# Optimization experiments

Measured on AMD Instinct MI355X. Metric: run time of the kernel, lower is better.

Reference implementation:

```python
import jax, jax.numpy as jnp
from jax import lax
import numpy as np

B, C, H, W = 4, 256, 64, 64
CQK = C // 8  # 32


def conv3x3(x, w, b):
    # x: [B,C_in,H,W], w: [C_out,C_in,3,3], b: [C_out]
    y = lax.conv_general_dilated(x, w, window_strides=(1, 1), padding='SAME',
                                 dimension_numbers=('NCHW', 'OIHW', 'NCHW'))
    return y + b[None, :, None, None]


def setup_inputs() -> dict:
    key = jax.random.key(0)
    ks = jax.random.split(key, 8)
    scale = 0.02
    return {
        'x': jax.random.normal(ks[0], (B, C, H, W), dtype=jnp.float32),
        'wq': jax.random.normal(ks[1], (CQK, C, 3, 3), dtype=jnp.float32) * scale,
        'bq': jax.random.normal(ks[2], (CQK,), dtype=jnp.float32) * scale,
        'wk': jax.random.normal(ks[3], (CQK, C, 3, 3), dtype=jnp.float32) * scale,
        'bk': jax.random.normal(ks[4], (CQK,), dtype=jnp.float32) * scale,
        'wv': jax.random.normal(ks[5], (C, C, 3, 3), dtype=jnp.float32) * scale,
        'bv': jax.random.normal(ks[6], (C,), dtype=jnp.float32) * scale,
        'gamma': jax.random.normal(ks[7], (1,), dtype=jnp.float32) * scale,
    }


def reference(x, wq, bq, wk, bk, wv, bv, gamma):
    b, c, h, w = x.shape
    n = h * w
    # Q: [B, N, C//8]  (permute(0,2,1) of the flattened conv output)
    q = conv3x3(x, wq, bq).reshape(b, -1, n).transpose(0, 2, 1)
    # K: [B, C//8, N]
    k = conv3x3(x, wk, bk).reshape(b, -1, n)
    # s: [B, N_q, N_k]
    s = jnp.einsum('bqd,bdk->bqk', q, k)
    # NOTE: original uses Softmax(dim=-2), i.e. over the QUERY axis
    attn_T = jax.nn.softmax(s, axis=-2)
    # V: [B, C, N]
    v = conv3x3(x, wv, bv).reshape(b, c, n)
    # o = bmm(V, attn_T): [B, C, N]
    o = jnp.einsum('bcq,bqk->bck', v, attn_T).reshape(b, c, h, w)
    return x + gamma * o
```

## Files before the change

### kernel.cpp

```cpp
#include <hip/hip_runtime.h>
#include <cstddef>

#define N_PIX 4096
#define HW 64
#define LOG2E 1.4426950408889634f
#define SHIFT2 28.8539008177793f

typedef __attribute__((ext_vector_type(8))) short bf16x8;
typedef __attribute__((ext_vector_type(4))) float f32x4;

static __device__ __forceinline__ unsigned short f2bf(float f) {
    union { float f; unsigned u; } v; v.f = f;
    unsigned r = v.u + 0x7fffu + ((v.u >> 16) & 1u);
    return (unsigned short)(r >> 16);
}
static __device__ __forceinline__ float bf2f(unsigned short s) {
    union { unsigned u; float f; } v; v.u = (unsigned)s << 16;
    return v.f;
}
static __device__ __forceinline__ unsigned pack_bf16_trunc(float lo, float hi) {
    union { float f; unsigned u; } a, b; a.f = hi; b.f = lo;
    return __builtin_amdgcn_perm(a.u, b.u, 0x07060302u);
}

__global__ __launch_bounds__(256) void x_transpose(
    const float* __restrict__ x, unsigned short* __restrict__ xbf)
{
    __shared__ unsigned short Ts[64][72];
    const int tid = threadIdx.x;
    const int px0 = blockIdx.x * 64, ci0 = blockIdx.y * 64, b = blockIdx.z;
    const float* xb = x + ((size_t)b * 256 + ci0) * N_PIX;

#pragma unroll
    for (int r = 0; r < 4; ++r) {
        int c = r * 16 + (tid >> 4);
        int p4 = (tid & 15) * 4;
        float4 v = *(const float4*)&xb[(size_t)c * N_PIX + px0 + p4];
        Ts[c][p4 + 0] = f2bf(v.x);
        Ts[c][p4 + 1] = f2bf(v.y);
        Ts[c][p4 + 2] = f2bf(v.z);
        Ts[c][p4 + 3] = f2bf(v.w);
    }
    __syncthreads();
#pragma unroll
    for (int r = 0; r < 2; ++r) {
        int id = tid * 2 + r;
        int p = id >> 3, c8 = (id & 7) * 8;
        ushort4 lo, hi;
        lo.x = Ts[c8 + 0][p]; lo.y = Ts[c8 + 1][p];
        lo.z = Ts[c8 + 2][p]; lo.w = Ts[c8 + 3][p];
        hi.x = Ts[c8 + 4][p]; hi.y = Ts[c8 + 5][p];
        hi.z = Ts[c8 + 6][p]; hi.w = Ts[c8 + 7][p];
        size_t off = ((size_t)b * N_PIX + px0 + p) * 256 + ci0 + c8;
        *(ushort4*)&xbf[off]     = lo;
        *(ushort4*)&xbf[off + 4] = hi;
    }
}

__global__ __launch_bounds__(256) void w_transform(
    const float* __restrict__ wq, const float* __restrict__ wk,
    const float* __restrict__ wv, unsigned short* __restrict__ wAll)
{
    int gid = blockIdx.x * 256 + threadIdx.x;
    if (gid >= 72 * 320 * 4) return;
    int part = gid & 3;
    int m = (gid >> 2) % 320;
    int kb = gid / 1280;
    int t = kb >> 3;
    int ci0 = (kb & 7) * 32 + part * 8;
    const float* src; int co; float sc = 1.f;
    if (m < 256)      { src = wv; co = m; }
    else if (m < 288) { src = wq; co = m - 256; sc = LOG2E; }
    else              { src = wk; co = m - 288; }
    ushort4 lo, hi;
    lo.x = f2bf(sc * src[((size_t)co * 256 + ci0 + 0) * 9 + t]);
    lo.y = f2bf(sc * src[((size_t)co * 256 + ci0 + 1) * 9 + t]);
    lo.z = f2bf(sc * src[((size_t)co * 256 + ci0 + 2) * 9 + t]);
    lo.w = f2bf(sc * src[((size_t)co * 256 + ci0 + 3) * 9 + t]);
    hi.x = f2bf(sc * src[((size_t)co * 256 + ci0 + 4) * 9 + t]);
    hi.y = f2bf(sc * src[((size_t)co * 256 + ci0 + 5) * 9 + t]);
    hi.z = f2bf(sc * src[((size_t)co * 256 + ci0 + 6) * 9 + t]);
    hi.w = f2bf(sc * src[((size_t)co * 256 + ci0 + 7) * 9 + t]);
    size_t off = ((size_t)kb * 320 + m) * 32 + part * 8;
    *(ushort4*)&wAll[off]     = lo;
    *(ushort4*)&wAll[off + 4] = hi;
}

__global__ __launch_bounds__(512, 2) void conv_gemm_v5(
    const unsigned short* __restrict__ xbf, const unsigned short* __restrict__ wAll,
    const float* __restrict__ bq, const float* __restrict__ bk,
    const float* __restrict__ bv,
    unsigned short* __restrict__ vbf, unsigned short* __restrict__ qt,
    unsigned short* __restrict__ kt)
{
    __shared__ unsigned short Xs[3 * 66 * 136];

    const int tid = threadIdx.x;
    const int w = tid >> 6, lane = tid & 63, quad = lane >> 4, l15 = lane & 15;
    const int y = blockIdx.x;
    const int b = blockIdx.y;
    const int r0 = (w >> 1) * 80;
    const int p0 = (w & 1) * 32;

    const unsigned short* xb = xbf + (size_t)b * N_PIX * 256;
    const unsigned short* aBase = wAll + ((size_t)(r0 + l15) * 32 + quad * 8);

    const int scol = tid >> 3;
    const int sg2  = (tid & 7) * 2;

    bf16x8 S[3][2];
    auto stage_load = [&](int h) {
#pragma unroll
        for (int ry = 0; ry < 3; ++ry) {
            int gy = y + ry - 1;
            if ((unsigned)gy < 64u) {
                const unsigned short* s =
                    xb + ((size_t)(gy * 64 + scol) * 256 + h * 128 + sg2 * 8);
                S[ry][0] = *(const bf16x8*)&s[0];
                S[ry][1] = *(const bf16x8*)&s[8];
            } else {
                S[ry][0] = (bf16x8){0,0,0,0,0,0,0,0};
                S[ry][1] = (bf16x8){0,0,0,0,0,0,0,0};
            }
        }
    };
    auto stage_store = [&]() {
#pragma unroll
        for (int ry = 0; ry < 3; ++ry) {
            *(bf16x8*)&Xs[(ry * 66 + scol + 1) * 136 + sg2 * 8]     = S[ry][0];
            *(bf16x8*)&Xs[(ry * 66 + scol + 1) * 136 + sg2 * 8 + 8] = S[ry][1];
        }
    };

    bf16x8 afA[2][5], afB[2][5];
    auto load_a = [&](int kb, bf16x8 (&af)[2][5]) {
        const unsigned short* p = aBase + (size_t)kb * 10240;
#pragma unroll
        for (int kl = 0; kl < 2; ++kl)
#pragma unroll
            for (int cb = 0; cb < 5; ++cb)
                af[kl][cb] = *(const bf16x8*)&p[kl * 10240 + cb * 512];
    };

    bf16x8 bfA[2][2], bfB[2][2];
    auto load_bf = [&](int t, int q2, bf16x8 (&bf)[2][2]) {
        int ty = t / 3;
        int dx = t - ty * 3 - 1;
#pragma unroll
        for (int kl = 0; kl < 2; ++kl)
#pragma unroll
            for (int jb = 0; jb < 2; ++jb) {
                int sx = p0 + jb * 16 + l15 + dx + 1;
                int cg = q2 * 8 + kl * 4 + quad;
                bf[kl][jb] = *(const bf16x8*)&Xs[(ty * 66 + sx) * 136 + cg * 8];
            }
    };

    f32x4 acc[5][2];
#pragma unroll
    for (int cb = 0; cb < 5; ++cb)
#pragma unroll
        for (int jb = 0; jb < 2; ++jb) acc[cb][jb] = (f32x4){0.f, 0.f, 0.f, 0.f};

    auto mfma_step = [&](bf16x8 (&af)[2][5], bf16x8 (&bf)[2][2]) {
#pragma unroll
        for (int kl = 0; kl < 2; ++kl)
#pragma unroll
            for (int cb = 0; cb < 5; ++cb)
#pragma unroll
                for (int jb = 0; jb < 2; ++jb)
                    acc[cb][jb] = __builtin_amdgcn_mfma_f32_16x16x32_bf16(
                        af[kl][cb], bf[kl][jb], acc[cb][jb], 0, 0, 0);
    };

    stage_load(0);
    load_a(0, afA);
    stage_store();
    if (tid < 96) {
        int ry = tid >> 5, rem = tid & 31;
        int sx = (rem >> 4) ? 65 : 0;
        int cg = rem & 15;
        *(bf16x8*)&Xs[(ry * 66 + sx) * 136 + cg * 8] = (bf16x8){0,0,0,0,0,0,0,0};
    }
    __syncthreads();

    stage_load(1);

    load_bf(0, 0, bfA);
#pragma unroll
    for (int s = 0; s < 18; s += 2) {
        const int t1 = (s + 1) >> 1, q1 = (s + 1) & 1;
        load_a(t1 * 8 + q1 * 2, afB);
        load_bf(t1, q1, bfB);
        mfma_step(afA, bfA);
        if (s + 2 < 18) {
            const int t2 = (s + 2) >> 1, q2_ = (s + 2) & 1;
            load_a(t2 * 8 + q2_ * 2, afA);
            load_bf(t2, q2_, bfA);
        } else {
            load_a(4, afA);
        }
        mfma_step(afB, bfB);
    }

    __syncthreads();
    stage_store();
    __syncthreads();

    load_bf(0, 0, bfA);
#pragma unroll
    for (int s = 0; s < 18; s += 2) {
        const int t1 = (s + 1) >> 1, q1 = (s + 1) & 1;
        load_a(t1 * 8 + 4 + q1 * 2, afB);
        load_bf(t1, q1, bfB);
        mfma_step(afA, bfA);
        if (s + 2 < 18) {
            const int t2 = (s + 2) >> 1, q2_ = (s + 2) & 1;
            load_a(t2 * 8 + 4 + q2_ * 2, afA);
            load_bf(t2, q2_, bfA);
        }
        mfma_step(afB, bfB);
    }

#pragma unroll
    for (int cb = 0; cb < 5; ++cb) {
        int cBase = r0 + cb * 16 + quad * 4;
#pragma unroll
        for (int r = 0; r < 4; ++r) {
            int c = cBase + r;
            if (c < 256) {
                float bias = bv[c];
#pragma unroll
                for (int jb = 0; jb < 2; ++jb) {
                    int px = y * 64 + p0 + jb * 16 + l15;
                    vbf[((size_t)b * 256 + c) * N_PIX + px] = f2bf(acc[cb][jb][r] + bias);
                }
            } else if (c < 288) {
                float bias = bq[c - 256] * LOG2E;
#pragma unroll
                for (int jb = 0; jb < 2; ++jb) {
                    int px = y * 64 + p0 + jb * 16 + l15;
                    qt[((size_t)b * N_PIX + px) * 32 + (c - 256)] = f2bf(acc[cb][jb][r] + bias);
                }
            } else {
                float bias = bk[c - 288];
#pragma unroll
                for (int jb = 0; jb < 2; ++jb) {
                    int px = y * 64 + p0 + jb * 16 + l15;
                    kt[((size_t)b * N_PIX + px) * 32 + (c - 288)] = f2bf(acc[cb][jb][r] + bias);
                }
            }
        }
    }
}

__global__ __launch_bounds__(256, 2) void fused_attn_mfma(
    const unsigned short* __restrict__ qt, const unsigned short* __restrict__ kt,
    const unsigned short* __restrict__ vbf,
    unsigned short* __restrict__ Abuf, float* __restrict__ lbuf, int iRange)
{
    const int tid  = threadIdx.x;
    const int w    = tid >> 6;
    const int lane = tid & 63;
    const int quad = lane >> 4;
    const int l15  = lane & 15;
    const int j0   = blockIdx.x * 128;
    const int b    = blockIdx.y;
    const int sp   = blockIdx.z;
    const int iBeg = sp * iRange;
    const int NI   = iRange / 64;

    const unsigned short* qtb = qt + (size_t)b * N_PIX * 32;
    const unsigned short* ktb = kt + (size_t)b * N_PIX * 32;
    const unsigned short* vb  = vbf + (size_t)b * 256 * N_PIX;

    __shared__ unsigned Pfrag[2][4096];
    __shared__ float lred[4][128];

    bf16x8 kf[8];
#pragma unroll
    for (int jb = 0; jb < 8; ++jb)
        kf[jb] = *(const bf16x8*)&ktb[((size_t)(j0 + jb * 16 + l15)) * 32 + quad * 8];

    f32x4 acc[4][8];
#pragma unroll
    for (int cb = 0; cb < 4; ++cb)
#pragma unroll
        for (int jb = 0; jb < 8; ++jb)
            acc[cb][jb] = (f32x4){0.f, 0.f, 0.f, 0.f};

    float lpart[8] = {0.f, 0.f, 0.f, 0.f, 0.f, 0.f, 0.f, 0.f};

    const int wFrag = w >> 1;
    const int wL    = ((w & 1) << 5) + ((quad >> 1) << 4) + l15;
    const int wEl2  = (quad & 1) << 1;

    bf16x8 va[2][4];

    auto s_phase = [&](bf16x8 qa, int buf) {
#pragma unroll
        for (int jb = 0; jb < 8; ++jb) {
            f32x4 s = __builtin_amdgcn_mfma_f32_16x16x32_bf16(
                qa, kf[jb], (f32x4){-SHIFT2, -SHIFT2, -SHIFT2, -SHIFT2}, 0, 0, 0);
            float p0 = __builtin_amdgcn_exp2f(s[0]);
            float p1 = __builtin_amdgcn_exp2f(s[1]);
            float p2 = __builtin_amdgcn_exp2f(s[2]);
            float p3 = __builtin_amdgcn_exp2f(s[3]);
            lpart[jb] += (p0 + p1) + (p2 + p3);
            unsigned u0 = pack_bf16_trunc(p0, p1);
            unsigned u1 = pack_bf16_trunc(p2, p3);
            unsigned base = (((jb << 1) + wFrag) * 64 + wL) * 4 + wEl2;
            Pfrag[buf][base]     = u0;
            Pfrag[buf][base + 1] = u1;
        }
    };

    auto load_qa = [&](int i0) {
        return *(const bf16x8*)&qtb[((size_t)(i0 + w * 16 + l15)) * 32 + quad * 8];
    };
    auto load_va = [&](int i0) {
#pragma unroll
        for (int ks = 0; ks < 2; ++ks)
#pragma unroll
            for (int cb = 0; cb < 4; ++cb)
                va[ks][cb] = *(const bf16x8*)&vb[((size_t)(w * 64 + cb * 16 + l15)) * N_PIX
                                                 + i0 + ks * 32 + quad * 8];
    };

    load_va(iBeg);
    s_phase(load_qa(iBeg), 0);

    for (int n = 0; n < NI; ++n) {
        __syncthreads();
        const bool hasN = (n + 1 < NI);
        const int inext = iBeg + (n + 1) * 64;
        bf16x8 qaN;
        if (hasN) qaN = load_qa(inext);

#pragma unroll
        for (int ks = 0; ks < 2; ++ks) {
            bf16x8 pb[8];
#pragma unroll
            for (int jb = 0; jb < 8; ++jb)
                pb[jb] = *(const bf16x8*)&Pfrag[n & 1][(((jb << 1) + ks) * 64 + lane) * 4];
#pragma unroll
            for (int cb = 0; cb < 4; ++cb)
#pragma unroll
                for (int jb = 0; jb < 8; ++jb)
                    acc[cb][jb] = __builtin_amdgcn_mfma_f32_16x16x32_bf16(
                        va[ks][cb], pb[jb], acc[cb][jb], 0, 0, 0);
        }

        if (hasN) {
            load_va(inext);
            s_phase(qaN, (n + 1) & 1);
        }
    }

#pragma unroll
    for (int jb = 0; jb < 8; ++jb) {
        float v = lpart[jb];
        v += __shfl_xor(v, 16, 64);
        v += __shfl_xor(v, 32, 64);
        lpart[jb] = v;
    }
    if (lane < 16) {
#pragma unroll
        for (int jb = 0; jb < 8; ++jb)
            lred[w][jb * 16 + l15] = lpart[jb];
    }
    __syncthreads();
    if (tid < 128) {
        float s = lred[0][tid] + lred[1][tid] + lred[2][tid] + lred[3][tid];
        lbuf[((size_t)sp * 4 + b) * N_PIX + j0 + tid] = s;
    }

    unsigned short* Ab = Abuf + ((size_t)sp * 4 + b) * 256 * N_PIX;
#pragma unroll
    for (int cb = 0; cb < 4; ++cb) {
        int c = w * 64 + cb * 16 + quad * 4;
#pragma unroll
        for (int jb = 0; jb < 8; ++jb) {
            int j = j0 + jb * 16 + l15;
#pragma unroll
            for (int r = 0; r < 4; ++r)
                Ab[(size_t)(c + r) * N_PIX + j] = f2bf(acc[cb][jb][r]);
        }
    }
}

__global__ __launch_bounds__(256) void combine_kernel(
    const unsigned short* __restrict__ A, const float* __restrict__ L,
    const float* __restrict__ x, const float* __restrict__ gamma,
    float* __restrict__ out, int split)
{
    const size_t CH = (size_t)4 * 256 * N_PIX;
    size_t flat = ((size_t)blockIdx.x * 256 + threadIdx.x) * 8;
    int j = (int)(flat & (N_PIX - 1));
    int b = (int)(flat >> 20);

    float a[8] = {0.f, 0.f, 0.f, 0.f, 0.f, 0.f, 0.f, 0.f};
    float l[8] = {0.f, 0.f, 0.f, 0.f, 0.f, 0.f, 0.f, 0.f};
    for (int s = 0; s < split; ++s) {
        ushort4 av0 = *(const ushort4*)&A[flat + (size_t)s * CH];
        ushort4 av1 = *(const ushort4*)&A[flat + (size_t)s * CH + 4];
        a[0] += bf2f(av0.x); a[1] += bf2f(av0.y); a[2] += bf2f(av0.z); a[3] += bf2f(av0.w);
        a[4] += bf2f(av1.x); a[5] += bf2f(av1.y); a[6] += bf2f(av1.z); a[7] += bf2f(av1.w);
        float4 l0 = *(const float4*)&L[((size_t)s * 4 + b) * N_PIX + j];
        float4 l1 = *(const float4*)&L[((size_t)s * 4 + b) * N_PIX + j + 4];
        l[0] += l0.x; l[1] += l0.y; l[2] += l0.z; l[3] += l0.w;
        l[4] += l1.x; l[5] += l1.y; l[6] += l1.z; l[7] += l1.w;
    }
    float g = gamma[0];
    float4 x0 = *(const float4*)&x[flat];
    float4 x1 = *(const float4*)&x[flat + 4];
    float4 o0, o1;
    o0.x = x0.x + g * a[0] / l[0];
    o0.y = x0.y + g * a[1] / l[1];
    o0.z = x0.z + g * a[2] / l[2];
    o0.w = x0.w + g * a[3] / l[3];
    o1.x = x1.x + g * a[4] / l[4];
    o1.y = x1.y + g * a[5] / l[5];
    o1.z = x1.z + g * a[6] / l[6];
    o1.w = x1.w + g * a[7] / l[7];
    *(float4*)&out[flat]     = o0;
    *(float4*)&out[flat + 4] = o1;
}

extern "C" void kernel_launch(void* const* d_in, const int* in_sizes, int n_in,
                              void* d_out, int out_size, void* d_ws, size_t ws_size,
                              hipStream_t stream)
{
    const float* x     = (const float*)d_in[0];
    const float* wq    = (const float*)d_in[1];
    const float* bq    = (const float*)d_in[2];
    const float* wk    = (const float*)d_in[3];
    const float* bk    = (const float*)d_in[4];
    const float* wv    = (const float*)d_in[5];
    const float* bv    = (const float*)d_in[6];
    const float* gamma = (const float*)d_in[7];
    float* out = (float*)d_out;

    const size_t szQTel  = (size_t)4 * N_PIX * 32;
    const size_t szVBFel = (size_t)4 * 256 * N_PIX;
    const size_t szXBFel = (size_t)4 * N_PIX * 256;
    const size_t szWel   = (size_t)72 * 320 * 32;
    const size_t fixedB  = (2 * szQTel + szVBFel + szXBFel + szWel) * 2;

    int split = 4;
    while (split > 1) {
        size_t need = fixedB
                    + (size_t)split * 4 * 256 * N_PIX * 2
                    + (size_t)split * 4 * N_PIX * 4;
        if (need <= ws_size) break;
        split >>= 1;
    }

    unsigned short* Abuf = (unsigned short*)d_ws;
    float* lbuf = (float*)(Abuf + (size_t)split * 4 * 256 * N_PIX);
    unsigned short* qt   = (unsigned short*)(lbuf + (size_t)split * 4 * N_PIX);
    unsigned short* kt   = qt + szQTel;
    unsigned short* vbf  = kt + szQTel;
    unsigned short* xbf  = vbf + szVBFel;
    unsigned short* wAll = xbf + szXBFel;

    x_transpose<<<dim3(N_PIX / 64, 4, 4), 256, 0, stream>>>(x, xbf);
    w_transform<<<dim3((72 * 320 * 4 + 255) / 256), 256, 0, stream>>>(wq, wk, wv, wAll);

    conv_gemm_v5<<<dim3(HW, 4), 512, 0, stream>>>(
        xbf, wAll, bq, bk, bv, vbf, qt, kt);

    fused_attn_mfma<<<dim3(N_PIX / 128, 4, split), 256, 0, stream>>>(
        qt, kt, vbf, Abuf, lbuf, N_PIX / split);

    combine_kernel<<<dim3((4 * 256 * N_PIX) / (256 * 8)), 256, 0, stream>>>(
        Abuf, lbuf, x, gamma, out, split);
}
```

Baseline: 197.3 us.

## Rewrite conv GEMM with direct global-to-LDS loads and triple-buffered pipeline

```diff
diff --git a/kernel.cpp b/kernel.cpp
--- a/kernel.cpp
+++ b/kernel.cpp
@@ -8,6 +8,7 @@
 
 typedef __attribute__((ext_vector_type(8))) short bf16x8;
 typedef __attribute__((ext_vector_type(4))) float f32x4;
+typedef unsigned int u32;
 
 static __device__ __forceinline__ unsigned short f2bf(float f) {
     union { float f; unsigned u; } v; v.f = f;
@@ -21,6 +22,11 @@
 static __device__ __forceinline__ unsigned pack_bf16_trunc(float lo, float hi) {
     union { float f; unsigned u; } a, b; a.f = hi; b.f = lo;
     return __builtin_amdgcn_perm(a.u, b.u, 0x07060302u);
+}
+static __device__ __forceinline__ void gll16(const void* g, void* l) {
+    __builtin_amdgcn_global_load_lds(
+        (const __attribute__((address_space(1))) u32*)g,
+        (__attribute__((address_space(3))) u32*)l, 16, 0, 0);
 }
 
 __global__ __launch_bounds__(256) void x_transpose(
@@ -59,9 +65,11 @@
 
 __global__ __launch_bounds__(256) void w_transform(
     const float* __restrict__ wq, const float* __restrict__ wk,
-    const float* __restrict__ wv, unsigned short* __restrict__ wAll)
+    const float* __restrict__ wv, unsigned short* __restrict__ wAll,
+    unsigned short* __restrict__ zp)
 {
     int gid = blockIdx.x * 256 + threadIdx.x;
+    if (gid < 256) zp[gid] = 0;
     if (gid >= 72 * 320 * 4) return;
     int part = gid & 3;
     int m = (gid >> 2) % 320;
@@ -86,75 +94,54 @@
     *(ushort4*)&wAll[off + 4] = hi;
 }
 
-__global__ __launch_bounds__(512, 2) void conv_gemm_v5(
+__global__ __launch_bounds__(256, 2) void conv_gemm_v6(
     const unsigned short* __restrict__ xbf, const unsigned short* __restrict__ wAll,
     const float* __restrict__ bq, const float* __restrict__ bk,
-    const float* __restrict__ bv,
+    const float* __restrict__ bv, const unsigned short* __restrict__ zpage,
     unsigned short* __restrict__ vbf, unsigned short* __restrict__ qt,
     unsigned short* __restrict__ kt)
 {
-    __shared__ unsigned short Xs[3 * 66 * 136];
+    __shared__ unsigned short Bl[3 * 7168];
 
     const int tid = threadIdx.x;
     const int w = tid >> 6, lane = tid & 63, quad = lane >> 4, l15 = lane & 15;
-    const int y = blockIdx.x;
-    const int b = blockIdx.y;
-    const int r0 = (w >> 1) * 80;
-    const int p0 = (w & 1) * 32;
+    const int y = blockIdx.x, rh = blockIdx.y, b = blockIdx.z;
+    const int rg = w >> 1;
+    const int pxh = w & 1;
 
     const unsigned short* xb = xbf + (size_t)b * N_PIX * 256;
-    const unsigned short* aBase = wAll + ((size_t)(r0 + l15) * 32 + quad * 8);
-
-    const int scol = tid >> 3;
-    const int sg2  = (tid & 7) * 2;
-
-    bf16x8 S[3][2];
-    auto stage_load = [&](int h) {
-#pragma unroll
-        for (int ry = 0; ry < 3; ++ry) {
-            int gy = y + ry - 1;
-            if ((unsigned)gy < 64u) {
-                const unsigned short* s =
-                    xb + ((size_t)(gy * 64 + scol) * 256 + h * 128 + sg2 * 8);
-                S[ry][0] = *(const bf16x8*)&s[0];
-                S[ry][1] = *(const bf16x8*)&s[8];
+    const unsigned short* aSrc = wAll + (size_t)rh * 160 * 32;
+
+    auto stage = [&](int kb, int buf) {
+        const int t_ = kb >> 3;
+        const int ty = t_ / 3;
+        const int dy = ty - 1, dx = t_ - ty * 3 - 1;
+        const int gy = y + dy;
+        const bool rowOK = ((unsigned)gy < 64u);
+        const int ci0 = (kb & 7) * 32;
+        const unsigned short* aS = aSrc + (size_t)kb * 10240;
+        unsigned short* tile = &Bl[buf * 7168];
+#pragma unroll
+        for (int r = 0; r < 4; ++r) {
+            const int c = r * 4 + w;
+            if (r == 3 && w >= 2) continue;
+            if (c < 10) {
+                int o = c * 1024 + lane * 16;
+                int u = o ^ (((o >> 7) & 7) << 4);
+                gll16(aS + (u >> 1), tile + c * 512);
             } else {
-                S[ry][0] = (bf16x8){0,0,0,0,0,0,0,0};
-                S[ry][1] = (bf16x8){0,0,0,0,0,0,0,0};
+                int o = (c - 10) * 1024 + lane * 16;
+                int u = o ^ (((o >> 7) & 7) << 4);
+                int px = u >> 6, k16 = (u >> 4) & 3;
+                int gx = px + dx;
+                const unsigned short* src =
+                    (rowOK && (unsigned)gx < 64u)
+                        ? xb + ((size_t)(gy * 64 + gx) * 256 + ci0 + k16 * 8)
+                        : zpage;
+                gll16(src, tile + 5120 + (c - 10) * 512);
             }
         }
     };
-    auto stage_store = [&]() {
-#pragma unroll
-        for (int ry = 0; ry < 3; ++ry) {
-            *(bf16x8*)&Xs[(ry * 66 + scol + 1) * 136 + sg2 * 8]     = S[ry][0];
-            *(bf16x8*)&Xs[(ry * 66 + scol + 1) * 136 + sg2 * 8 + 8] = S[ry][1];
-        }
-    };
-
-    bf16x8 afA[2][5], afB[2][5];
-    auto load_a = [&](int kb, bf16x8 (&af)[2][5]) {
-        const unsigned short* p = aBase + (size_t)kb * 10240;
-#pragma unroll
-        for (int kl = 0; kl < 2; ++kl)
-#pragma unroll
-            for (int cb = 0; cb < 5; ++cb)
-                af[kl][cb] = *(const bf16x8*)&p[kl * 10240 + cb * 512];
-    };
-
-    bf16x8 bfA[2][2], bfB[2][2];
-    auto load_bf = [&](int t, int q2, bf16x8 (&bf)[2][2]) {
-        int ty = t / 3;
-        int dx = t - ty * 3 - 1;
-#pragma unroll
-        for (int kl = 0; kl < 2; ++kl)
-#pragma unroll
-            for (int jb = 0; jb < 2; ++jb) {
-                int sx = p0 + jb * 16 + l15 + dx + 1;
-                int cg = q2 * 8 + kl * 4 + quad;
-                bf[kl][jb] = *(const bf16x8*)&Xs[(ty * 66 + sx) * 136 + cg * 8];
-            }
-    };
 
     f32x4 acc[5][2];
 #pragma unroll
@@ -162,69 +149,62 @@
 #pragma unroll
         for (int jb = 0; jb < 2; ++jb) acc[cb][jb] = (f32x4){0.f, 0.f, 0.f, 0.f};
 
-    auto mfma_step = [&](bf16x8 (&af)[2][5], bf16x8 (&bf)[2][2]) {
-#pragma unroll
-        for (int kl = 0; kl < 2; ++kl)
-#pragma unroll
-            for (int cb = 0; cb < 5; ++cb)
-#pragma unroll
-                for (int jb = 0; jb < 2; ++jb)
-                    acc[cb][jb] = __builtin_amdgcn_mfma_f32_16x16x32_bf16(
-                        af[kl][cb], bf[kl][jb], acc[cb][jb], 0, 0, 0);
-    };
-
-    stage_load(0);
-    load_a(0, afA);
-    stage_store();
-    if (tid < 96) {
-        int ry = tid >> 5, rem = tid & 31;
-        int sx = (rem >> 4) ? 65 : 0;
-        int cg = rem & 15;
-        *(bf16x8*)&Xs[(ry * 66 + sx) * 136 + cg * 8] = (bf16x8){0,0,0,0,0,0,0,0};
-    }
-    __syncthreads();
-
-    stage_load(1);
-
-    load_bf(0, 0, bfA);
-#pragma unroll
-    for (int s = 0; s < 18; s += 2) {
-        const int t1 = (s + 1) >> 1, q1 = (s + 1) & 1;
-        load_a(t1 * 8 + q1 * 2, afB);
-        load_bf(t1, q1, bfB);
-        mfma_step(afA, bfA);
-        if (s + 2 < 18) {
-            const int t2 = (s + 2) >> 1, q2_ = (s + 2) & 1;
-            load_a(t2 * 8 + q2_ * 2, afA);
-            load_bf(t2, q2_, bfA);
-        } else {
-            load_a(4, afA);
-        }
-        mfma_step(afB, bfB);
-    }
-
-    __syncthreads();
-    stage_store();
-    __syncthreads();
-
-    load_bf(0, 0, bfA);
-#pragma unroll
-    for (int s = 0; s < 18; s += 2) {
-        const int t1 = (s + 1) >> 1, q1 = (s + 1) & 1;
-        load_a(t1 * 8 + 4 + q1 * 2, afB);
-        load_bf(t1, q1, bfB);
-        mfma_step(afA, bfA);
-        if (s + 2 < 18) {
-            const int t2 = (s + 2) >> 1, q2_ = (s + 2) & 1;
-            load_a(t2 * 8 + 4 + q2_ * 2, afA);
-            load_bf(t2, q2_, bfA);
-        }
-        mfma_step(afB, bfB);
+    stage(0, 0);
+    stage(1, 1);
+    if (w < 2) asm volatile("s_waitcnt vmcnt(4)" ::: "memory");
+    else       asm volatile("s_waitcnt vmcnt(3)" ::: "memory");
+    __builtin_amdgcn_s_barrier();
+    __builtin_amdgcn_sched_barrier(0);
+
+    int buf = 0;
+    for (int kb = 0; kb < 72; ++kb) {
+        int nb = buf + 1; if (nb == 3) nb = 0;
+        int pb = nb + 1;  if (pb == 3) pb = 0;
+        const bool more2 = (kb + 2 < 72);
+        const bool more1 = (kb + 1 < 72);
+        if (more2) stage(kb + 2, pb);
+
+        const int bb = buf * 7168;
+        bf16x8 af[5], bfr[2];
+#pragma unroll
+        for (int cb = 0; cb < 5; ++cb) {
+            int sr = rg * 80 + cb * 16 + l15;
+            int u = sr * 64 + quad * 16;
+            u ^= ((u >> 7) & 7) << 4;
+            af[cb] = *(const bf16x8*)&Bl[bb + (u >> 1)];
+        }
+#pragma unroll
+        for (int jb = 0; jb < 2; ++jb) {
+            int px = pxh * 32 + jb * 16 + l15;
+            int u = px * 64 + quad * 16;
+            u ^= ((u >> 7) & 7) << 4;
+            bfr[jb] = *(const bf16x8*)&Bl[bb + 5120 + (u >> 1)];
+        }
+        __builtin_amdgcn_s_setprio(1);
+#pragma unroll
+        for (int cb = 0; cb < 5; ++cb)
+#pragma unroll
+            for (int jb = 0; jb < 2; ++jb)
+                acc[cb][jb] = __builtin_amdgcn_mfma_f32_16x16x32_bf16(
+                    af[cb], bfr[jb], acc[cb][jb], 0, 0, 0);
+        __builtin_amdgcn_s_setprio(0);
+
+        if (more2) {
+            if (w < 2) asm volatile("s_waitcnt vmcnt(4)" ::: "memory");
+            else       asm volatile("s_waitcnt vmcnt(3)" ::: "memory");
+        } else if (more1) {
+            asm volatile("s_waitcnt vmcnt(0)" ::: "memory");
+        }
+        if (more1) {
+            __builtin_amdgcn_s_barrier();
+            __builtin_amdgcn_sched_barrier(0);
+        }
+        buf = nb;
     }
 
 #pragma unroll
     for (int cb = 0; cb < 5; ++cb) {
-        int cBase = r0 + cb * 16 + quad * 4;
+        int cBase = rh * 160 + rg * 80 + cb * 16 + quad * 4;
 #pragma unroll
         for (int r = 0; r < 4; ++r) {
             int c = cBase + r;
@@ -232,21 +212,21 @@
                 float bias = bv[c];
 #pragma unroll
                 for (int jb = 0; jb < 2; ++jb) {
-                    int px = y * 64 + p0 + jb * 16 + l15;
+                    int px = y * 64 + pxh * 32 + jb * 16 + l15;
                     vbf[((size_t)b * 256 + c) * N_PIX + px] = f2bf(acc[cb][jb][r] + bias);
                 }
             } else if (c < 288) {
                 float bias = bq[c - 256] * LOG2E;
 #pragma unroll
                 for (int jb = 0; jb < 2; ++jb) {
-                    int px = y * 64 + p0 + jb * 16 + l15;
+                    int px = y * 64 + pxh * 32 + jb * 16 + l15;
                     qt[((size_t)b * N_PIX + px) * 32 + (c - 256)] = f2bf(acc[cb][jb][r] + bias);
                 }
             } else {
                 float bias = bk[c - 288];
 #pragma unroll
                 for (int jb = 0; jb < 2; ++jb) {
-                    int px = y * 64 + p0 + jb * 16 + l15;
+                    int px = y * 64 + pxh * 32 + jb * 16 + l15;
                     kt[((size_t)b * N_PIX + px) * 32 + (c - 288)] = f2bf(acc[cb][jb][r] + bias);
                 }
             }
@@ -445,7 +425,7 @@
     const size_t szVBFel = (size_t)4 * 256 * N_PIX;
     const size_t szXBFel = (size_t)4 * N_PIX * 256;
     const size_t szWel   = (size_t)72 * 320 * 32;
-    const size_t fixedB  = (2 * szQTel + szVBFel + szXBFel + szWel) * 2;
+    const size_t fixedB  = (2 * szQTel + szVBFel + szXBFel + szWel + 256) * 2;
 
     int split = 4;
     while (split > 1) {
@@ -458,17 +438,19 @@
 
     unsigned short* Abuf = (unsigned short*)d_ws;
     float* lbuf = (float*)(Abuf + (size_t)split * 4 * 256 * N_PIX);
-    unsigned short* qt   = (unsigned short*)(lbuf + (size_t)split * 4 * N_PIX);
-    unsigned short* kt   = qt + szQTel;
-    unsigned short* vbf  = kt + szQTel;
-    unsigned short* xbf  = vbf + szVBFel;
-    unsigned short* wAll = xbf + szXBFel;
+    unsigned short* qt    = (unsigned short*)(lbuf + (size_t)split * 4 * N_PIX);
+    unsigned short* kt    = qt + szQTel;
+    unsigned short* vbf   = kt + szQTel;
+    unsigned short* xbf   = vbf + szVBFel;
+    unsigned short* wAll  = xbf + szXBFel;
+    unsigned short* zpage = wAll + szWel;
 
     x_transpose<<<dim3(N_PIX / 64, 4, 4), 256, 0, stream>>>(x, xbf);
-    w_transform<<<dim3((72 * 320 * 4 + 255) / 256), 256, 0, stream>>>(wq, wk, wv, wAll);
-
-    conv_gemm_v5<<<dim3(HW, 4), 512, 0, stream>>>(
-        xbf, wAll, bq, bk, bv, vbf, qt, kt);
+    w_transform<<<dim3((72 * 320 * 4 + 255) / 256), 256, 0, stream>>>(
+        wq, wk, wv, wAll, zpage);
+
+    conv_gemm_v6<<<dim3(HW, 2, 4), 256, 0, stream>>>(
+        xbf, wAll, bq, bk, bv, zpage, vbf, qt, kt);
 
     fused_attn_mfma<<<dim3(N_PIX / 128, 4, split), 256, 0, stream>>>(
         qt, kt, vbf, Abuf, lbuf, N_PIX / split);
```

Result: faster. 178.7 us (-9.4%).
